# Performance work log

Hardware: AMD Instinct MI355X
Metric: run time of the kernel (lower is better)

## Reference

```python
import jax, jax.numpy as jnp
import numpy as np

B = 1024
D = 128  # in_out_dim


def _lin(k, i, o):
    return jax.random.normal(k, (i, o), jnp.float32) / np.sqrt(i)


def setup_inputs() -> dict:
    key = jax.random.key(0)
    ks = jax.random.split(key, 24)
    inp = {
        'pseudo_t': jax.random.uniform(ks[0], (), jnp.float32),
        'x': jax.random.normal(ks[1], (B, D), jnp.float32),
        'g_x': jax.random.normal(ks[2], (B, 1), jnp.float32),
        'p': jax.random.uniform(ks[3], (B, 1), jnp.float32),
        # GRN encoder: 128->1024->960->896 (Tanh), decoder 896->128
        'gw0': _lin(ks[4], 128, 1024), 'gb0': jnp.zeros((1024,), jnp.float32),
        'gw1': _lin(ks[5], 1024, 960), 'gb1': jnp.zeros((960,), jnp.float32),
        'gw2': _lin(ks[6], 960, 896), 'gb2': jnp.zeros((896,), jnp.float32),
        'gdw': _lin(ks[7], 896, 128), 'gdb': jnp.zeros((128,), jnp.float32),
        # BRD encoder: 129->512->448 (Tanh), decoder 448->1
        'bw0': _lin(ks[8], 129, 512), 'bb0': jnp.zeros((512,), jnp.float32),
        'bw1': _lin(ks[9], 512, 448), 'bb1': jnp.zeros((448,), jnp.float32),
        'bdw': _lin(ks[10], 448, 1), 'bdb': jnp.zeros((1,), jnp.float32),
    }
    return inp


def reference(pseudo_t, x, g_x, p, gw0, gb0, gw1, gb1, gw2, gb2, gdw, gdb,
              bw0, bb0, bw1, bb1, bdw, bdb):
    bsz = x.shape[0]
    x_gene = x[:, :-1]                       # [B, D-1]
    s = jnp.full((bsz, 1), pseudo_t, x.dtype)

    def grn(state):                          # [..., D] -> [..., D]
        h = jnp.tanh(state @ gw0 + gb0)
        h = jnp.tanh(h @ gw1 + gb1)
        h = jnp.tanh(h @ gw2 + gb2)
        return h @ gdw + gdb

    dx_dt = grn(jnp.concatenate([s, x_gene], axis=1))   # [B, D]

    # BRD growth function g(x, t)
    st = jnp.concatenate([s, x], axis=1)                # [B, D+1]
    e = jnp.tanh(st @ bw0 + bb0)
    e = jnp.tanh(e @ bw1 + bb1)
    g = e @ bdw + bdb                                   # [B, 1]

    # trace of d(dx_dt[:, :D-1]) / d(x_gene), per sample (CNF divergence)
    s_scalar = jnp.reshape(pseudo_t, (1,)).astype(x.dtype)

    def f_single(xg_i):                                 # [D-1] -> [D]
        return grn(jnp.concatenate([s_scalar, xg_i]))

    jac = jax.vmap(jax.jacfwd(f_single))(x_gene)        # [B, D, D-1]
    tr = jnp.trace(jac[:, :D - 1, :], axis1=1, axis2=2) # [B]

    dp_dt = g - p * tr[:, None]                         # [B, 1]
    return (dx_dt, g, dp_dt)
```

## Files before the change

### kernel.cpp

```cpp
#include <hip/hip_runtime.h>


typedef __bf16 bf16;
typedef __bf16 bf16x8 __attribute__((ext_vector_type(8)));
typedef float floatx4 __attribute__((ext_vector_type(4)));

#if defined(__has_builtin)
#if __has_builtin(__builtin_amdgcn_global_load_lds)
#define HAVE_GLL 1
#endif
#endif

typedef __attribute__((address_space(3))) char lds_char_t;
typedef __attribute__((address_space(1))) const char gbl_char_t;

__device__ inline void async_load16(const void* gp, void* lp) {
#ifdef HAVE_GLL
  __builtin_amdgcn_global_load_lds((gbl_char_t*)gp, (lds_char_t*)lp, 16, 0, 0);
#else
  *(bf16x8*)lp = *(const bf16x8*)gp;
#endif
}

__device__ inline void stage_async(const bf16* src, long row0, int ld, int kc,
                                   bf16* dst, int wid, int sr8, int cph) {
#pragma unroll
  for (int t = 0; t < 4; ++t) {
    const int r = (wid * 4 + t) * 8 + sr8;
    const int csrc = (cph - r) & 7;
    async_load16(src + (row0 + r) * (size_t)ld + kc + csrc * 8,
                 dst + r * 64 + cph * 8);
  }
}

__device__ inline void mfma_block(const bf16* As, const bf16* Bs,
                                  floatx4 (&acc)[4][4], int wm, int wn,
                                  int l16, int quad) {
#pragma unroll
  for (int ks = 0; ks < 2; ++ks) {
    bf16x8 af[4], bfv[4];
#pragma unroll
    for (int mt = 0; mt < 4; ++mt) {
      const int r = wm * 64 + mt * 16 + l16;
      const int c = (ks * 4 + quad + r) & 7;
      af[mt] = *(const bf16x8*)(As + r * 64 + c * 8);
    }
#pragma unroll
    for (int nt = 0; nt < 4; ++nt) {
      const int r = wn * 64 + nt * 16 + l16;
      const int c = (ks * 4 + quad + r) & 7;
      bfv[nt] = *(const bf16x8*)(Bs + r * 64 + c * 8);
    }
#pragma unroll
    for (int mt = 0; mt < 4; ++mt)
#pragma unroll
      for (int nt = 0; nt < 4; ++nt)
        acc[mt][nt] = __builtin_amdgcn_mfma_f32_16x16x32_bf16(af[mt], bfv[nt], acc[mt][nt], 0, 0, 0);
  }
}

struct TArgs {
  const bf16* A;
  const bf16* B;
  const bf16* d1b;
  bf16* Upr;
  const bf16* d2b;
  const float* gdw;
  float* tr;
  int i0; int K; int ch;
};

template <int MODE>
__global__ __launch_bounds__(256, 4) void kt_tile(TArgs p) {
  const int idx = blockIdx.x;
  const int mt8 = (idx >> 3) & 7;
  const int nb  = ((idx >> 6) << 3) + (idx & 7);
  if (nb >= p.ch) return;
  if (MODE == 1 && mt8 == 7) return;

  __shared__ __align__(16) char lds[34816];
  bf16* As = (bf16*)lds;
  bf16* Bs = As + 8192;
  bf16* bounce = (bf16*)lds;
  __shared__ float red4[4];

  const int tid  = threadIdx.x;
  const int wid  = tid >> 6, lane = tid & 63;
  const int wm   = wid & 1, wn = wid >> 1;
  const int quad = lane >> 4, l16 = lane & 15;
  const int sr8  = lane >> 3, cph = lane & 7;
  const int m0   = mt8 * 128;
  const int ig   = p.i0 + nb;
  const int n0   = nb * 128;

  floatx4 acc[4][4];
#pragma unroll
  for (int a = 0; a < 4; ++a)
#pragma unroll
    for (int b = 0; b < 4; ++b)
#pragma unroll
      for (int r = 0; r < 4; ++r) acc[a][b][r] = 0.0f;

  for (int kc = 0; kc < p.K; kc += 64) {
    stage_async(p.A, m0, 1024, kc, As, wid, sr8, cph);
    stage_async(p.B, n0, 1024, kc, Bs, wid, sr8, cph);
    __syncthreads();
    mfma_block(As, Bs, acc, wm, wn, l16, quad);
    __syncthreads();
  }

  if (MODE == 0) {
#pragma unroll
    for (int nt = 0; nt < 4; ++nt) {
      const int nl = wn * 64 + nt * 16 + l16;
#pragma unroll
      for (int mt = 0; mt < 4; ++mt)
#pragma unroll
        for (int r = 0; r < 4; ++r) {
          const int ml = wm * 64 + mt * 16 + quad * 4 + r;
          const int mg = m0 + ml;
          const float d1v = (mg < 960) ? (float)p.d1b[(size_t)ig * 960 + mg] : 0.0f;
          bounce[nl * 136 + ml] = (bf16)(acc[mt][nt][r] * d1v);
        }
    }
    __syncthreads();
    const int r2 = tid >> 1, half16 = tid & 1;
    const int chLim = (mt8 == 7) ? 8 : 16;
#pragma unroll
    for (int c = 0; c < 8; ++c) {
      const int ch16 = half16 * 8 + c;
      if (ch16 < chLim) {
        bf16x8 v = *(const bf16x8*)(bounce + r2 * 136 + ch16 * 8);
        *(bf16x8*)(p.Upr + (size_t)(n0 + r2) * 1024 + m0 + ch16 * 8) = v;
      }
    }
  } else {
    float s = 0.0f;
#pragma unroll
    for (int nt = 0; nt < 4; ++nt) {
      const int d = wn * 64 + nt * 16 + l16;
      if (d < 127) {
#pragma unroll
        for (int mt = 0; mt < 4; ++mt)
#pragma unroll
          for (int r = 0; r < 4; ++r) {
            const int mg = m0 + wm * 64 + mt * 16 + quad * 4 + r;
            const float w = (float)p.d2b[(size_t)ig * 896 + mg] * p.gdw[mg * 128 + d];
            s += acc[mt][nt][r] * w;
          }
      }
    }
#pragma unroll
    for (int off = 1; off < 64; off <<= 1) s += __shfl_xor(s, off, 64);
    if (lane == 0) red4[wid] = s;
    __syncthreads();
    if (tid == 0) atomicAdd(p.tr + ig, red4[0] + red4[1] + red4[2] + red4[3]);
  }
}

struct FArgs {
  const bf16* A; int lda;
  const bf16* Bt; int ldb;
  const float* bias;
  bf16* C; int ldc;
  bf16* D; int ldd;
  float* outF; int ldo;
  int K; int realN;
};

template <int ACT>
__global__ __launch_bounds__(256) void kt_fwd(FArgs p) {
  __shared__ __align__(16) bf16 As[8192];
  __shared__ __align__(16) bf16 Bs[8192];
  const int tid  = threadIdx.x;
  const int wid  = tid >> 6, lane = tid & 63;
  const int wm   = wid & 1, wn = wid >> 1;
  const int quad = lane >> 4, l16 = lane & 15;
  const int sr8  = lane >> 3, cph = lane & 7;
  const int m0   = blockIdx.x * 128;
  const int bn0  = blockIdx.y * 128;

  floatx4 acc[4][4];
#pragma unroll
  for (int a = 0; a < 4; ++a)
#pragma unroll
    for (int b = 0; b < 4; ++b)
#pragma unroll
      for (int r = 0; r < 4; ++r) acc[a][b][r] = 0.0f;

  for (int kc = 0; kc < p.K; kc += 64) {
    stage_async(p.A, m0, p.lda, kc, As, wid, sr8, cph);
    stage_async(p.Bt, bn0, p.ldb, kc, Bs, wid, sr8, cph);
    __syncthreads();
    mfma_block(As, Bs, acc, wm, wn, l16, quad);
    __syncthreads();
  }

#pragma unroll
  for (int nt = 0; nt < 4; ++nt) {
    const int ng = bn0 + wn * 64 + nt * 16 + l16;
    const float bv = (ng < p.realN) ? p.bias[ng] : 0.0f;
#pragma unroll
    for (int mt = 0; mt < 4; ++mt)
#pragma unroll
      for (int r = 0; r < 4; ++r) {
        const int i = m0 + wm * 64 + mt * 16 + quad * 4 + r;
        const float v = acc[mt][nt][r] + bv;
        if (ACT) {
          const float t = tanhf(v);
          p.C[(size_t)i * p.ldc + ng] = (ng < p.realN) ? (bf16)t : (bf16)0.0f;
          if (p.D && ng < p.realN)
            p.D[(size_t)i * p.ldd + ng] = (bf16)(1.0f - t * t);
        } else if (ng < p.realN) {
          p.outF[(size_t)i * p.ldo + ng] = v;
        }
      }
  }
}

struct PArgs {
  const float *gw0, *gw1, *gw2, *gdw, *bw0, *bw1, *pt, *x;
  bf16 *gw0b, *gw0t, *gw1t, *gw2t, *gdwt, *bw0t, *bw1t, *Xg, *Xb;
};

__device__ inline void tpose_tile(bf16* dst, const float* src, int R, int C,
                                  int ldd, int tile, int tilesX, float* tl,
                                  int tid) {
  const int r0 = (tile % tilesX) * 64;
  const int c0 = (tile / tilesX) * 64;
  const int tx = tid & 63, ty0 = tid >> 6;
#pragma unroll
  for (int i = 0; i < 16; ++i) {
    const int ty = ty0 + i * 4;
    const int r = r0 + ty, c = c0 + tx;
    tl[ty * 65 + tx] = (r < R && c < C) ? src[(size_t)r * C + c] : 0.0f;
  }
  __syncthreads();
#pragma unroll
  for (int i = 0; i < 16; ++i) {
    const int ty = ty0 + i * 4;
    dst[(size_t)(c0 + ty) * ldd + r0 + tx] = (bf16)tl[tx * 65 + ty];
  }
}

__global__ __launch_bounds__(256) void kt_prep(PArgs p) {
  __shared__ float tl[64 * 65];
  int b = blockIdx.x;
  const int t = threadIdx.x;
  if (b < 512) { p.gw0b[b * 256 + t] = (bf16)p.gw0[b * 256 + t]; return; }
  b -= 512;
  if (b < 768) {
    const int idx = b * 256 + t;
    const int i = idx / 192, c = idx % 192;
    const float s = p.pt[0];
    float vb;
    if (c == 0) vb = s;
    else if (c <= 128) vb = p.x[i * 128 + c - 1];
    else vb = 0.0f;
    p.Xb[i * 192 + c] = (bf16)vb;
    if (c < 128) p.Xg[i * 128 + c] = (bf16)((c == 0) ? s : p.x[i * 128 + c - 1]);
    return;
  }
  b -= 768;
  if (b < 32)  { tpose_tile(p.gw0t, p.gw0, 128, 1024, 128, b, 2, tl, t);  return; }
  b -= 32;
  if (b < 256) { tpose_tile(p.gw1t, p.gw1, 1024, 960, 1024, b, 16, tl, t); return; }
  b -= 256;
  if (b < 256) { tpose_tile(p.gw2t, p.gw2, 960, 896, 1024, b, 16, tl, t); return; }
  b -= 256;
  if (b < 32)  { tpose_tile(p.gdwt, p.gdw, 896, 128, 1024, b, 16, tl, t); return; }
  b -= 32;
  if (b < 24)  { tpose_tile(p.bw0t, p.bw0, 129, 512, 192, b, 3, tl, t);  return; }
  b -= 24;
  if (b < 64)  { tpose_tile(p.bw1t, p.bw1, 512, 448, 512, b, 8, tl, t);  return; }
}

__global__ __launch_bounds__(256) void kt_g0(bf16* G0, const bf16* gw0b,
                                             const bf16* d0b, int i0, int ch) {
  const int b = blockIdx.x;
  const int nb = ((b >> 9) << 3) + (b & 7);
  const int inner = (b >> 3) & 63;
  if (nb >= ch) return;
  const int e = inner * 256 + threadIdx.x;
  const int d = e >> 7;
  const int j = (e & 127) << 3;
  const int ig = i0 + nb;
  const int wsel = (d + 1 < 128) ? d + 1 : 127;
  bf16x8 gv = *(const bf16x8*)(gw0b + wsel * 1024 + j);
  bf16x8 dv = *(const bf16x8*)(d0b + (size_t)ig * 1024 + j);
  bf16x8 v;
#pragma unroll
  for (int k = 0; k < 8; ++k) v[k] = (bf16)((float)gv[k] * (float)dv[k]);
  *(bf16x8*)(G0 + ((size_t)nb * 128 + d) * 1024 + j) = v;
}

__global__ __launch_bounds__(256) void kt_gdot(const bf16* e1b, const float* bdw,
                                               const float* bdb, float* gf, float* gout) {
  const int i = blockIdx.x * 4 + (threadIdx.x >> 6);
  const int lane = threadIdx.x & 63;
  float s = 0.0f;
  for (int k = lane; k < 448; k += 64) s += (float)e1b[(size_t)i * 512 + k] * bdw[k];
#pragma unroll
  for (int off = 32; off > 0; off >>= 1) s += __shfl_down(s, off, 64);
  if (lane == 0) {
    const float v = s + bdb[0];
    gf[i] = v;
    gout[i] = v;
  }
}

__global__ __launch_bounds__(256) void kt_fin(const float* gf, const float* tr,
                                              const float* pp, float* dp) {
  const int i = blockIdx.x * 256 + threadIdx.x;
  if (i < 1024) dp[i] = gf[i] - pp[i] * tr[i];
}

extern "C" void kernel_launch(void* const* d_in, const int* in_sizes, int n_in,
                              void* d_out, int out_size, void* d_ws, size_t ws_size,
                              hipStream_t stream) {
  const float* pt  = (const float*)d_in[0];
  const float* x   = (const float*)d_in[1];
  const float* pp  = (const float*)d_in[3];
  const float* gw0 = (const float*)d_in[4];
  const float* gb0 = (const float*)d_in[5];
  const float* gw1 = (const float*)d_in[6];
  const float* gb1 = (const float*)d_in[7];
  const float* gw2 = (const float*)d_in[8];
  const float* gb2 = (const float*)d_in[9];
  const float* gdw = (const float*)d_in[10];
  const float* gdb = (const float*)d_in[11];
  const float* bw0 = (const float*)d_in[12];
  const float* bb0 = (const float*)d_in[13];
  const float* bw1 = (const float*)d_in[14];
  const float* bb1 = (const float*)d_in[15];
  const float* bdw = (const float*)d_in[16];
  const float* bdb = (const float*)d_in[17];
  float* out = (float*)d_out;

  char* w = (char*)d_ws;
  size_t used = 0;
  auto alloc = [&](size_t nbytes) -> void* {
    void* r = w + used;
    used += (nbytes + 255) & ~(size_t)255;
    return r;
  };
  bf16* gw0b = (bf16*)alloc((size_t)128 * 1024 * 2);
  bf16* gw0t = (bf16*)alloc((size_t)1024 * 128 * 2);
  bf16* gw1t = (bf16*)alloc((size_t)1024 * 1024 * 2);
  bf16* gw2t = (bf16*)alloc((size_t)1024 * 1024 * 2);
  bf16* gdwt = (bf16*)alloc((size_t)128 * 1024 * 2);
  bf16* bw0t = (bf16*)alloc((size_t)512 * 192 * 2);
  bf16* bw1t = (bf16*)alloc((size_t)512 * 512 * 2);
  bf16* Xg   = (bf16*)alloc((size_t)1024 * 128 * 2);
  bf16* Xb   = (bf16*)alloc((size_t)1024 * 192 * 2);
  bf16* h0b  = (bf16*)alloc((size_t)1024 * 1024 * 2);
  bf16* h1b  = (bf16*)alloc((size_t)1024 * 1024 * 2);
  bf16* h2b  = (bf16*)alloc((size_t)1024 * 1024 * 2);
  bf16* e0b  = (bf16*)alloc((size_t)1024 * 512 * 2);
  bf16* e1b  = (bf16*)alloc((size_t)1024 * 512 * 2);
  bf16* d0b  = (bf16*)alloc((size_t)1024 * 1024 * 2);
  bf16* d1b  = (bf16*)alloc((size_t)1024 * 960 * 2);
  bf16* d2b  = (bf16*)alloc((size_t)1024 * 896 * 2);
  float* gf  = (float*)alloc(1024 * 4);
  float* tr  = (float*)alloc(1024 * 4);

  const size_t perSample = (size_t)128 * 1024 * 2;
  size_t avail = (ws_size > used) ? ws_size - used : 0;
  int CH = (int)(avail / (2 * perSample));
  if (CH > 256) CH = 256;
  if (CH < 1) CH = 1;
  bf16* G0  = (bf16*)alloc((size_t)CH * perSample);
  bf16* Upr = (bf16*)(w + used);

  hipMemsetAsync(tr, 0, 1024 * 4, stream);

  {
    PArgs a{gw0, gw1, gw2, gdw, bw0, bw1, pt, x,
            gw0b, gw0t, gw1t, gw2t, gdwt, bw0t, bw1t, Xg, Xb};
    kt_prep<<<dim3(1944), 256, 0, stream>>>(a);
  }

  {
    FArgs a{}; a.A = Xg; a.lda = 128; a.Bt = gw0t; a.ldb = 128; a.bias = gb0;
    a.C = h0b; a.ldc = 1024; a.D = d0b; a.ldd = 1024; a.K = 128; a.realN = 1024;
    kt_fwd<1><<<dim3(8, 8), 256, 0, stream>>>(a);
  }
  {
    FArgs a{}; a.A = h0b; a.lda = 1024; a.Bt = gw1t; a.ldb = 1024; a.bias = gb1;
    a.C = h1b; a.ldc = 1024; a.D = d1b; a.ldd = 960; a.K = 1024; a.realN = 960;
    kt_fwd<1><<<dim3(8, 8), 256, 0, stream>>>(a);
  }
  {
    FArgs a{}; a.A = h1b; a.lda = 1024; a.Bt = gw2t; a.ldb = 1024; a.bias = gb2;
    a.C = h2b; a.ldc = 1024; a.D = d2b; a.ldd = 896; a.K = 1024; a.realN = 896;
    kt_fwd<1><<<dim3(8, 7), 256, 0, stream>>>(a);
  }
  {
    FArgs a{}; a.A = h2b; a.lda = 1024; a.Bt = gdwt; a.ldb = 1024; a.bias = gdb;
    a.outF = out; a.ldo = 128; a.K = 896; a.realN = 128;
    kt_fwd<0><<<dim3(8, 1), 256, 0, stream>>>(a);
  }
  {
    FArgs a{}; a.A = Xb; a.lda = 192; a.Bt = bw0t; a.ldb = 192; a.bias = bb0;
    a.C = e0b; a.ldc = 512; a.K = 192; a.realN = 512;
    kt_fwd<1><<<dim3(8, 4), 256, 0, stream>>>(a);
  }
  {
    FArgs a{}; a.A = e0b; a.lda = 512; a.Bt = bw1t; a.ldb = 512; a.bias = bb1;
    a.C = e1b; a.ldc = 512; a.K = 512; a.realN = 448;
    kt_fwd<1><<<dim3(8, 4), 256, 0, stream>>>(a);
  }
  kt_gdot<<<dim3(256), 256, 0, stream>>>(e1b, bdw, bdb, gf, out + 131072);

  for (int i0 = 0; i0 < 1024; i0 += CH) {
    const int ch = (1024 - i0 < CH) ? (1024 - i0) : CH;
    const int ch8 = (ch + 7) & ~7;
    kt_g0<<<dim3(ch8 * 64), 256, 0, stream>>>(G0, gw0b, d0b, i0, ch);
    {
      TArgs a{}; a.A = gw1t; a.B = G0; a.d1b = d1b; a.Upr = Upr; a.i0 = i0;
      a.K = 1024; a.ch = ch;
      kt_tile<0><<<dim3(8 * ch8), 256, 0, stream>>>(a);
    }
    {
      TArgs a{}; a.A = gw2t; a.B = Upr; a.d2b = d2b; a.gdw = gdw; a.tr = tr;
      a.i0 = i0; a.K = 960; a.ch = ch;
      kt_tile<1><<<dim3(8 * ch8), 256, 0, stream>>>(a);
    }
  }

  kt_fin<<<dim3(4), 256, 0, stream>>>(gf, tr, pp, out + 132096);
}
```

Before: 896.3 us.

## Horizontally fuse independent forward GEMMs and G0 build into shared launches

Pairs of independent kernels now run as one launch, with blocks picking their job by block index. The GRN and BRD forward layers are paired, layer 2 of the GRN shares a launch with the first chunk's G0 construction, and the decoder GEMM shares one with the g dot product. Each chunk's second Jacobian GEMM also builds G0 for the next chunk, which drops a separate G0 launch per chunk. The aim is fewer launches and better GPU occupancy for small grids, at the cost of mixed block types whose resource use is set by the heavier body.

Result: faster. 793.1 us (-11.5%).

```diff
diff --git a/kernel.cpp b/kernel.cpp
--- a/kernel.cpp
+++ b/kernel.cpp
@@ -57,6 +57,24 @@
       for (int nt = 0; nt < 4; ++nt)
         acc[mt][nt] = __builtin_amdgcn_mfma_f32_16x16x32_bf16(af[mt], bfv[nt], acc[mt][nt], 0, 0, 0);
   }
+}
+
+__device__ inline void g0_body(bf16* G0, const bf16* gw0b, const bf16* d0b,
+                               int i0, int ch, int b, int tid) {
+  const int nb = ((b >> 9) << 3) + (b & 7);
+  const int inner = (b >> 3) & 63;
+  if (nb >= ch) return;
+  const int e = inner * 256 + tid;
+  const int d = e >> 7;
+  const int j = (e & 127) << 3;
+  const int ig = i0 + nb;
+  const int wsel = (d + 1 < 128) ? d + 1 : 127;
+  bf16x8 gv = *(const bf16x8*)(gw0b + wsel * 1024 + j);
+  bf16x8 dv = *(const bf16x8*)(d0b + (size_t)ig * 1024 + j);
+  bf16x8 v;
+#pragma unroll
+  for (int k = 0; k < 8; ++k) v[k] = (bf16)((float)gv[k] * (float)dv[k]);
+  *(bf16x8*)(G0 + ((size_t)nb * 128 + d) * 1024 + j) = v;
 }
 
 struct TArgs {
@@ -70,19 +88,16 @@
   int i0; int K; int ch;
 };
 
-template <int MODE>
-__global__ __launch_bounds__(256, 4) void kt_tile(TArgs p) {
+__global__ __launch_bounds__(256, 4) void kt_b1(TArgs p) {
   const int idx = blockIdx.x;
   const int mt8 = (idx >> 3) & 7;
   const int nb  = ((idx >> 6) << 3) + (idx & 7);
   if (nb >= p.ch) return;
-  if (MODE == 1 && mt8 == 7) return;
 
   __shared__ __align__(16) char lds[34816];
   bf16* As = (bf16*)lds;
   bf16* Bs = As + 8192;
   bf16* bounce = (bf16*)lds;
-  __shared__ float red4[4];
 
   const int tid  = threadIdx.x;
   const int wid  = tid >> 6, lane = tid & 63;
@@ -109,53 +124,96 @@
     __syncthreads();
   }
 
-  if (MODE == 0) {
-#pragma unroll
-    for (int nt = 0; nt < 4; ++nt) {
-      const int nl = wn * 64 + nt * 16 + l16;
+#pragma unroll
+  for (int nt = 0; nt < 4; ++nt) {
+    const int nl = wn * 64 + nt * 16 + l16;
+#pragma unroll
+    for (int mt = 0; mt < 4; ++mt)
+#pragma unroll
+      for (int r = 0; r < 4; ++r) {
+        const int ml = wm * 64 + mt * 16 + quad * 4 + r;
+        const int mg = m0 + ml;
+        const float d1v = (mg < 960) ? (float)p.d1b[(size_t)ig * 960 + mg] : 0.0f;
+        bounce[nl * 136 + ml] = (bf16)(acc[mt][nt][r] * d1v);
+      }
+  }
+  __syncthreads();
+  const int r2 = tid >> 1, half16 = tid & 1;
+  const int chLim = (mt8 == 7) ? 8 : 16;
+#pragma unroll
+  for (int c = 0; c < 8; ++c) {
+    const int ch16 = half16 * 8 + c;
+    if (ch16 < chLim) {
+      bf16x8 v = *(const bf16x8*)(bounce + r2 * 136 + ch16 * 8);
+      *(bf16x8*)(p.Upr + (size_t)(n0 + r2) * 1024 + m0 + ch16 * 8) = v;
+    }
+  }
+}
+
+__global__ __launch_bounds__(256, 4) void kt_b2g0(TArgs p, int nB2,
+                                                  bf16* G0n, const bf16* gw0b,
+                                                  const bf16* d0b, int i0n, int chn) {
+  __shared__ __align__(16) char lds[34816];
+  __shared__ float red4[4];
+  const int tid = threadIdx.x;
+  const int idx = blockIdx.x;
+
+  if (idx >= nB2) {
+    if (chn > 0) g0_body(G0n, gw0b, d0b, i0n, chn, idx - nB2, tid);
+    return;
+  }
+
+  const int mt8 = (idx >> 3) & 7;
+  const int nb  = ((idx >> 6) << 3) + (idx & 7);
+  if (nb >= p.ch || mt8 == 7) return;
+
+  bf16* As = (bf16*)lds;
+  bf16* Bs = As + 8192;
+
+  const int wid  = tid >> 6, lane = tid & 63;
+  const int wm   = wid & 1, wn = wid >> 1;
+  const int quad = lane >> 4, l16 = lane & 15;
+  const int sr8  = lane >> 3, cph = lane & 7;
+  const int m0   = mt8 * 128;
+  const int ig   = p.i0 + nb;
+  const int n0   = nb * 128;
+
+  floatx4 acc[4][4];
+#pragma unroll
+  for (int a = 0; a < 4; ++a)
+#pragma unroll
+    for (int b = 0; b < 4; ++b)
+#pragma unroll
+      for (int r = 0; r < 4; ++r) acc[a][b][r] = 0.0f;
+
+  for (int kc = 0; kc < p.K; kc += 64) {
+    stage_async(p.A, m0, 1024, kc, As, wid, sr8, cph);
+    stage_async(p.B, n0, 1024, kc, Bs, wid, sr8, cph);
+    __syncthreads();
+    mfma_block(As, Bs, acc, wm, wn, l16, quad);
+    __syncthreads();
+  }
+
+  float s = 0.0f;
+#pragma unroll
+  for (int nt = 0; nt < 4; ++nt) {
+    const int d = wn * 64 + nt * 16 + l16;
+    if (d < 127) {
 #pragma unroll
       for (int mt = 0; mt < 4; ++mt)
 #pragma unroll
         for (int r = 0; r < 4; ++r) {
-          const int ml = wm * 64 + mt * 16 + quad * 4 + r;
-          const int mg = m0 + ml;
-          const float d1v = (mg < 960) ? (float)p.d1b[(size_t)ig * 960 + mg] : 0.0f;
-          bounce[nl * 136 + ml] = (bf16)(acc[mt][nt][r] * d1v);
+          const int mg = m0 + wm * 64 + mt * 16 + quad * 4 + r;
+          const float w = (float)p.d2b[(size_t)ig * 896 + mg] * p.gdw[mg * 128 + d];
+          s += acc[mt][nt][r] * w;
         }
     }
-    __syncthreads();
-    const int r2 = tid >> 1, half16 = tid & 1;
-    const int chLim = (mt8 == 7) ? 8 : 16;
-#pragma unroll
-    for (int c = 0; c < 8; ++c) {
-      const int ch16 = half16 * 8 + c;
-      if (ch16 < chLim) {
-        bf16x8 v = *(const bf16x8*)(bounce + r2 * 136 + ch16 * 8);
-        *(bf16x8*)(p.Upr + (size_t)(n0 + r2) * 1024 + m0 + ch16 * 8) = v;
-      }
-    }
-  } else {
-    float s = 0.0f;
-#pragma unroll
-    for (int nt = 0; nt < 4; ++nt) {
-      const int d = wn * 64 + nt * 16 + l16;
-      if (d < 127) {
-#pragma unroll
-        for (int mt = 0; mt < 4; ++mt)
-#pragma unroll
-          for (int r = 0; r < 4; ++r) {
-            const int mg = m0 + wm * 64 + mt * 16 + quad * 4 + r;
-            const float w = (float)p.d2b[(size_t)ig * 896 + mg] * p.gdw[mg * 128 + d];
-            s += acc[mt][nt][r] * w;
-          }
-      }
-    }
-#pragma unroll
-    for (int off = 1; off < 64; off <<= 1) s += __shfl_xor(s, off, 64);
-    if (lane == 0) red4[wid] = s;
-    __syncthreads();
-    if (tid == 0) atomicAdd(p.tr + ig, red4[0] + red4[1] + red4[2] + red4[3]);
-  }
+  }
+#pragma unroll
+  for (int off = 1; off < 64; off <<= 1) s += __shfl_xor(s, off, 64);
+  if (lane == 0) red4[wid] = s;
+  __syncthreads();
+  if (tid == 0) atomicAdd(p.tr + ig, red4[0] + red4[1] + red4[2] + red4[3]);
 }
 
 struct FArgs {
@@ -165,20 +223,18 @@
   bf16* C; int ldc;
   bf16* D; int ldd;
   float* outF; int ldo;
-  int K; int realN;
+  int K; int realN; int gridX;
 };
 
 template <int ACT>
-__global__ __launch_bounds__(256) void kt_fwd(FArgs p) {
-  __shared__ __align__(16) bf16 As[8192];
-  __shared__ __align__(16) bf16 Bs[8192];
+__device__ inline void fwd_body(const FArgs& p, int bx, bf16* As, bf16* Bs) {
   const int tid  = threadIdx.x;
   const int wid  = tid >> 6, lane = tid & 63;
   const int wm   = wid & 1, wn = wid >> 1;
   const int quad = lane >> 4, l16 = lane & 15;
   const int sr8  = lane >> 3, cph = lane & 7;
-  const int m0   = blockIdx.x * 128;
-  const int bn0  = blockIdx.y * 128;
+  const int m0   = (bx % p.gridX) * 128;
+  const int bn0  = (bx / p.gridX) * 128;
 
   floatx4 acc[4][4];
 #pragma unroll
@@ -215,6 +271,45 @@
           p.outF[(size_t)i * p.ldo + ng] = v;
         }
       }
+  }
+}
+
+__global__ __launch_bounds__(256) void kt_fwd2(FArgs a, int na, FArgs b) {
+  __shared__ __align__(16) bf16 As[8192];
+  __shared__ __align__(16) bf16 Bs[8192];
+  const int bx = blockIdx.x;
+  if (bx < na) fwd_body<1>(a, bx, As, Bs);
+  else         fwd_body<1>(b, bx - na, As, Bs);
+}
+
+__global__ __launch_bounds__(256) void kt_l2g0(FArgs a, int na, bf16* G0,
+                                               const bf16* gw0b, const bf16* d0b,
+                                               int i0, int ch) {
+  __shared__ __align__(16) bf16 As[8192];
+  __shared__ __align__(16) bf16 Bs[8192];
+  const int bx = blockIdx.x;
+  if (bx < na) fwd_body<1>(a, bx, As, Bs);
+  else         g0_body(G0, gw0b, d0b, i0, ch, bx - na, threadIdx.x);
+}
+
+__global__ __launch_bounds__(256) void kt_dxgdot(FArgs a, int na,
+                                                 const bf16* e1b, const float* bdw,
+                                                 const float* bdb, float* gf,
+                                                 float* gout) {
+  __shared__ __align__(16) bf16 As[8192];
+  __shared__ __align__(16) bf16 Bs[8192];
+  const int bx = blockIdx.x;
+  if (bx < na) { fwd_body<0>(a, bx, As, Bs); return; }
+  const int i = (bx - na) * 4 + (threadIdx.x >> 6);
+  const int lane = threadIdx.x & 63;
+  float s = 0.0f;
+  for (int k = lane; k < 448; k += 64) s += (float)e1b[(size_t)i * 512 + k] * bdw[k];
+#pragma unroll
+  for (int off = 32; off > 0; off >>= 1) s += __shfl_down(s, off, 64);
+  if (lane == 0) {
+    const float v = s + bdb[0];
+    gf[i] = v;
+    gout[i] = v;
   }
 }
 
@@ -273,40 +368,6 @@
   if (b < 24)  { tpose_tile(p.bw0t, p.bw0, 129, 512, 192, b, 3, tl, t);  return; }
   b -= 24;
   if (b < 64)  { tpose_tile(p.bw1t, p.bw1, 512, 448, 512, b, 8, tl, t);  return; }
-}
-
-__global__ __launch_bounds__(256) void kt_g0(bf16* G0, const bf16* gw0b,
-                                             const bf16* d0b, int i0, int ch) {
-  const int b = blockIdx.x;
-  const int nb = ((b >> 9) << 3) + (b & 7);
-  const int inner = (b >> 3) & 63;
-  if (nb >= ch) return;
-  const int e = inner * 256 + threadIdx.x;
-  const int d = e >> 7;
-  const int j = (e & 127) << 3;
-  const int ig = i0 + nb;
-  const int wsel = (d + 1 < 128) ? d + 1 : 127;
-  bf16x8 gv = *(const bf16x8*)(gw0b + wsel * 1024 + j);
-  bf16x8 dv = *(const bf16x8*)(d0b + (size_t)ig * 1024 + j);
-  bf16x8 v;
-#pragma unroll
-  for (int k = 0; k < 8; ++k) v[k] = (bf16)((float)gv[k] * (float)dv[k]);
-  *(bf16x8*)(G0 + ((size_t)nb * 128 + d) * 1024 + j) = v;
-}
-
-__global__ __launch_bounds__(256) void kt_gdot(const bf16* e1b, const float* bdw,
-                                               const float* bdb, float* gf, float* gout) {
-  const int i = blockIdx.x * 4 + (threadIdx.x >> 6);
-  const int lane = threadIdx.x & 63;
-  float s = 0.0f;
-  for (int k = lane; k < 448; k += 64) s += (float)e1b[(size_t)i * 512 + k] * bdw[k];
-#pragma unroll
-  for (int off = 32; off > 0; off >>= 1) s += __shfl_down(s, off, 64);
-  if (lane == 0) {
-    const float v = s + bdb[0];
-    gf[i] = v;
-    gout[i] = v;
-  }
 }
 
 __global__ __launch_bounds__(256) void kt_fin(const float* gf, const float* tr,
@@ -383,48 +444,49 @@
   {
     FArgs a{}; a.A = Xg; a.lda = 128; a.Bt = gw0t; a.ldb = 128; a.bias = gb0;
     a.C = h0b; a.ldc = 1024; a.D = d0b; a.ldd = 1024; a.K = 128; a.realN = 1024;
-    kt_fwd<1><<<dim3(8, 8), 256, 0, stream>>>(a);
+    a.gridX = 8;
+    FArgs b{}; b.A = Xb; b.lda = 192; b.Bt = bw0t; b.ldb = 192; b.bias = bb0;
+    b.C = e0b; b.ldc = 512; b.K = 192; b.realN = 512; b.gridX = 8;
+    kt_fwd2<<<dim3(96), 256, 0, stream>>>(a, 64, b);
   }
   {
     FArgs a{}; a.A = h0b; a.lda = 1024; a.Bt = gw1t; a.ldb = 1024; a.bias = gb1;
     a.C = h1b; a.ldc = 1024; a.D = d1b; a.ldd = 960; a.K = 1024; a.realN = 960;
-    kt_fwd<1><<<dim3(8, 8), 256, 0, stream>>>(a);
-  }
+    a.gridX = 8;
+    FArgs b{}; b.A = e0b; b.lda = 512; b.Bt = bw1t; b.ldb = 512; b.bias = bb1;
+    b.C = e1b; b.ldc = 512; b.K = 512; b.realN = 448; b.gridX = 8;
+    kt_fwd2<<<dim3(96), 256, 0, stream>>>(a, 64, b);
+  }
+  const int ch0  = (1024 < CH) ? 1024 : CH;
+  const int ch08 = (ch0 + 7) & ~7;
   {
     FArgs a{}; a.A = h1b; a.lda = 1024; a.Bt = gw2t; a.ldb = 1024; a.bias = gb2;
     a.C = h2b; a.ldc = 1024; a.D = d2b; a.ldd = 896; a.K = 1024; a.realN = 896;
-    kt_fwd<1><<<dim3(8, 7), 256, 0, stream>>>(a);
+    a.gridX = 8;
+    kt_l2g0<<<dim3(56 + ch08 * 64), 256, 0, stream>>>(a, 56, G0, gw0b, d0b, 0, ch0);
   }
   {
     FArgs a{}; a.A = h2b; a.lda = 1024; a.Bt = gdwt; a.ldb = 1024; a.bias = gdb;
-    a.outF = out; a.ldo = 128; a.K = 896; a.realN = 128;
-    kt_fwd<0><<<dim3(8, 1), 256, 0, stream>>>(a);
-  }
-  {
-    FArgs a{}; a.A = Xb; a.lda = 192; a.Bt = bw0t; a.ldb = 192; a.bias = bb0;
-    a.C = e0b; a.ldc = 512; a.K = 192; a.realN = 512;
-    kt_fwd<1><<<dim3(8, 4), 256, 0, stream>>>(a);
-  }
-  {
-    FArgs a{}; a.A = e0b; a.lda = 512; a.Bt = bw1t; a.ldb = 512; a.bias = bb1;
-    a.C = e1b; a.ldc = 512; a.K = 512; a.realN = 448;
-    kt_fwd<1><<<dim3(8, 4), 256, 0, stream>>>(a);
-  }
-  kt_gdot<<<dim3(256), 256, 0, stream>>>(e1b, bdw, bdb, gf, out + 131072);
+    a.outF = out; a.ldo = 128; a.K = 896; a.realN = 128; a.gridX = 8;
+    kt_dxgdot<<<dim3(8 + 256), 256, 0, stream>>>(a, 8, e1b, bdw, bdb, gf, out + 131072);
+  }
 
   for (int i0 = 0; i0 < 1024; i0 += CH) {
-    const int ch = (1024 - i0 < CH) ? (1024 - i0) : CH;
+    const int ch  = (1024 - i0 < CH) ? (1024 - i0) : CH;
     const int ch8 = (ch + 7) & ~7;
-    kt_g0<<<dim3(ch8 * 64), 256, 0, stream>>>(G0, gw0b, d0b, i0, ch);
     {
       TArgs a{}; a.A = gw1t; a.B = G0; a.d1b = d1b; a.Upr = Upr; a.i0 = i0;
       a.K = 1024; a.ch = ch;
-      kt_tile<0><<<dim3(8 * ch8), 256, 0, stream>>>(a);
+      kt_b1<<<dim3(8 * ch8), 256, 0, stream>>>(a);
     }
     {
+      const int i0n = i0 + CH;
+      const int chn = (i0n < 1024) ? ((1024 - i0n < CH) ? (1024 - i0n) : CH) : 0;
+      const int chn8 = (chn + 7) & ~7;
       TArgs a{}; a.A = gw2t; a.B = Upr; a.d2b = d2b; a.gdw = gdw; a.tr = tr;
       a.i0 = i0; a.K = 960; a.ch = ch;
-      kt_tile<1><<<dim3(8 * ch8), 256, 0, stream>>>(a);
+      kt_b2g0<<<dim3(8 * ch8 + chn8 * 64), 256, 0, stream>>>(
+          a, 8 * ch8, G0, gw0b, d0b, i0n, chn);
     }
   }
 
```
